# Optimization experiments

Hardware: AMD Instinct MI355X
Metric: run time of the kernel (lower is better)

Reference implementation:

```python
import jax, jax.numpy as jnp
import numpy as np

SAMPLE_SIZE = 4096  # deterministic mode: first SAMPLE_SIZE flattened pixels
EPS_STD = 1e-8
EPS_PDF = 1e-10


def _std(v):
    # torch.std is unbiased (ddof=1)
    return jnp.std(v, ddof=1)


def _adaptive_sigma(v):
    # sigma=None path: 0.2 * std, clamped to [0.001, 1.0]
    return jnp.clip(_std(v) * 0.2, 0.001, 1.0)


def _normalize(v):
    return (v - jnp.mean(v)) / (_std(v) + EPS_STD)


def _marginal_pdf(values, sigma):
    vn = _normalize(values)                      # [N]
    resid = vn[None, :] - vn[:, None]            # [N, N]
    kernel = jnp.exp(-0.5 * (resid / sigma) ** 2)
    pdf = jnp.mean(kernel, axis=1)               # [N]
    return pdf / (jnp.sum(pdf) + EPS_PDF)


def _joint_pdf(v1, v2, s1, s2):
    vn1 = _normalize(v1)
    vn2 = _normalize(v2)
    r1 = vn1[None, :] - vn1[:, None]             # [N, N]
    r2 = vn2[None, :] - vn2[:, None]             # [N, N]
    kernel = jnp.exp(-0.5 * (r1 / s1) ** 2) * jnp.exp(-0.5 * (r2 / s2) ** 2)
    pdf = jnp.mean(kernel, axis=1)
    return pdf / (jnp.sum(pdf) + EPS_PDF)


def _mi_kde(img1, img2):
    x = img1.reshape(-1)[:SAMPLE_SIZE]
    y = img2.reshape(-1)[:SAMPLE_SIZE]
    s1 = _adaptive_sigma(x)
    s2 = _adaptive_sigma(y)
    p1 = _marginal_pdf(x, s1)
    p2 = _marginal_pdf(y, s2)
    pj = _joint_pdf(x, y, s1, s2)
    ratio = (pj + EPS_PDF) / (p1 * p2 + EPS_PDF)
    log_ratio = jnp.log(jnp.clip(ratio, 1e-10, 1e10))
    return jnp.sum(pj * log_ratio)


def setup_inputs() -> dict:
    key = jax.random.key(0)
    k1, k2, k3 = jax.random.split(key, 3)
    shape = (2, 1, 128, 128)  # [B, C, H, W] images in [0, 1]
    return {
        "fused_img": jax.random.uniform(k1, shape, dtype=jnp.float32),
        "source_img1": jax.random.uniform(k2, shape, dtype=jnp.float32),
        "source_img2": jax.random.uniform(k3, shape, dtype=jnp.float32),
    }


def reference(fused_img, source_img1, source_img2):
    B = fused_img.shape[0]
    total = jnp.float32(0.0)
    for b in range(B):  # small fixed batch loop, matches original
        total = total + _mi_kde(fused_img[b], source_img1[b]) \
                      + _mi_kde(fused_img[b], source_img2[b])
    return -(total / B)
```

## Files before the change

### kernel.cpp

```cpp
#include <hip/hip_runtime.h>

#define N 4096
#define NBIN 1024
#define LOG2E 1.4426950408889634f

__device__ __forceinline__ float fast_exp2(float x) {
#if __has_builtin(__builtin_amdgcn_exp2f)
    return __builtin_amdgcn_exp2f(x);
#else
    return exp2f(x);
#endif
}

__device__ float block_reduce_sum(float v) {
    __shared__ float red[16];
    int lane = threadIdx.x & 63;
    int wid = threadIdx.x >> 6;
    #pragma unroll
    for (int off = 32; off; off >>= 1) v += __shfl_down(v, off, 64);
    if (lane == 0) red[wid] = v;
    __syncthreads();
    if (threadIdx.x == 0) {
        int nw = (int)(blockDim.x >> 6);
        float s = red[0];
        for (int w = 1; w < nw; ++w) s += red[w];
        red[0] = s;
    }
    __syncthreads();
    float r = red[0];
    __syncthreads();
    return r;
}

__device__ float4 block_reduce_stats(float s, float sq, float mn, float mx) {
    __shared__ float4 red4[16];
    int lane = threadIdx.x & 63;
    int wid = threadIdx.x >> 6;
    #pragma unroll
    for (int off = 32; off; off >>= 1) {
        s  += __shfl_down(s, off, 64);
        sq += __shfl_down(sq, off, 64);
        mn  = fminf(mn, __shfl_down(mn, off, 64));
        mx  = fmaxf(mx, __shfl_down(mx, off, 64));
    }
    if (lane == 0) red4[wid] = make_float4(s, sq, mn, mx);
    __syncthreads();
    if (threadIdx.x == 0) {
        float4 r = red4[0];
        #pragma unroll
        for (int w = 1; w < 16; ++w) {
            float4 q = red4[w];
            r.x += q.x; r.y += q.y;
            r.z = fminf(r.z, q.z); r.w = fmaxf(r.w, q.w);
        }
        red4[0] = r;
    }
    __syncthreads();
    float4 r = red4[0];
    __syncthreads();
    return r;
}

__global__ void __launch_bounds__(1024)
k_prep(const float* __restrict__ fused,
       const float* __restrict__ s1,
       const float* __restrict__ s2,
       float2* __restrict__ xa,
       float2* __restrict__ ma,
       float* __restrict__ par,
       float* __restrict__ hcnt,
       float* __restrict__ hmu) {
    __shared__ unsigned int cnt[NBIN];
    __shared__ int qs[NBIN];
    int vec = blockIdx.x;
    int b = vec / 3, k = vec % 3;
    const float* src = (k == 0 ? fused : (k == 1 ? s1 : s2)) + b * 16384;
    int tid = threadIdx.x;

    cnt[tid] = 0u; qs[tid] = 0;

    float v[4];
    float s = 0.f, sq = 0.f, mn = 1e30f, mx = -1e30f;
    #pragma unroll
    for (int t = 0; t < 4; ++t) {
        v[t] = src[tid + t * 1024];
        s += v[t]; sq = fmaf(v[t], v[t], sq);
        mn = fminf(mn, v[t]); mx = fmaxf(mx, v[t]);
    }
    float4 r = block_reduce_stats(s, sq, mn, mx);
    float mean = r.x * (1.0f / 4096.0f);
    float tssq = r.y - 4096.0f * mean * mean;
    float stdv = sqrtf(fmaxf(tssq, 0.f) / 4095.0f);
    float sigma = fminf(fmaxf(0.2f * stdv, 0.001f), 1.0f);
    float inv = 1.0f / (stdv + 1e-8f);
    float c1 = -0.5f * LOG2E / (sigma * sigma);
    float xmin = (r.z - mean) * inv;
    float xmax = (r.w - mean) * inv;
    float range = fmaxf(xmax - xmin, 1e-6f);
    float inv_bw = (float)NBIN / range;
    float binw = range * (1.0f / NBIN);

    float2* xav = xa + (size_t)vec * N;
    float2* mav = ma + (size_t)vec * N;
    __syncthreads();
    #pragma unroll
    for (int t = 0; t < 4; ++t) {
        int i = tid + t * 1024;
        float x = (v[t] - mean) * inv;
        float a = c1 * x * x;
        xav[i] = make_float2(x, a);
        mav[i] = make_float2(-2.0f * c1 * x, a);
        float rel = x - xmin;
        int bb = min(NBIN - 1, max(0, (int)(rel * inv_bw)));
        atomicAdd(&cnt[bb], 1u);
        atomicAdd(&qs[bb], (int)rintf(rel * 16384.0f));
    }
    __syncthreads();
    {
        unsigned int c = cnt[tid];
        hcnt[vec * NBIN + tid] = (float)c;
        float mu = c ? xmin + ((float)qs[tid] / (float)c) * (1.0f / 16384.0f)
                     : xmin + (tid + 0.5f) * binw;
        hmu[vec * NBIN + tid] = mu;
    }
    if (tid == 0) {
        par[vec * 8 + 0] = xmin;
        par[vec * 8 + 1] = inv_bw;
        par[vec * 8 + 2] = binw;
        par[vec * 8 + 3] = c1;
    }
}

__global__ void __launch_bounds__(256, 8)
k_main(const float2* __restrict__ xa,
       const float2* __restrict__ ma,
       const float* __restrict__ par,
       const float* __restrict__ hcnt,
       const float* __restrict__ hmu,
       float* __restrict__ marg,
       float* __restrict__ msum_part,
       float* __restrict__ part, int js) {
    __shared__ float4 sj[128];
    const int nib = 4;
    int bid = blockIdx.x;
    int tid = threadIdx.x;

    if (bid < 96) {
        int vec = bid >> 4, ic = bid & 15;
        int i = ic * 256 + tid;
        const float* P = par + vec * 8;
        float xmin = P[0], inv_bw = P[1], c1 = P[3];
        float xi = xa[(size_t)vec * N + i].x;
        float R = sqrtf(45.0f / fabsf(c1));
        int b0 = max(0, (int)((xi - R - xmin) * inv_bw));
        int b1 = min(NBIN - 1, (int)((xi + R - xmin) * inv_bw) + 1);
        const float* hc = hcnt + vec * NBIN;
        const float* hm = hmu + vec * NBIN;
        float acc = 0.f;
        #pragma unroll 4
        for (int bb = b0; bb <= b1; ++bb) {
            float d = xi - hm[bb];
            acc += hc[bb] * fast_exp2(c1 * d * d);
        }
        float raw = acc * (1.0f / N);
        marg[(size_t)vec * N + i] = raw;
        float tot = block_reduce_sum(raw);
        if (tid == 0) msum_part[bid] = tot;
        return;
    }

    int bid2 = bid - 96;
    int tt = bid2 / (nib * js);
    int rem = bid2 % (nib * js);
    int ib = rem / js, jsp = rem % js;
    int b = tt >> 1, pr = tt & 1;
    int vx = b * 3, vy = b * 3 + 1 + pr;
    int jlen = N / js;
    int j0 = jsp * jlen;
    int ibase = ib * 1024 + tid;

    const float2* xav = xa + (size_t)vx * N;
    const float2* yav = xa + (size_t)vy * N;
    const float2* mxv = ma + (size_t)vx * N;
    const float2* myv = ma + (size_t)vy * N;

    float mx[4], my[4], C[4];
    #pragma unroll
    for (int u = 0; u < 4; ++u) {
        float2 qx = mxv[ibase + u * 256];
        float2 qy = myv[ibase + u * 256];
        mx[u] = qx.x; my[u] = qy.x; C[u] = qx.y + qy.y;
    }
    float acc[4] = {0.f, 0.f, 0.f, 0.f};

    for (int jt = 0; jt < jlen; jt += 128) {
        int cnt = min(128, jlen - jt);
        __syncthreads();
        if (tid < cnt) {
            float2 xq = xav[j0 + jt + tid];
            float2 yq = yav[j0 + jt + tid];
            sj[tid] = make_float4(xq.x, yq.x, xq.y + yq.y, 0.f);
        }
        __syncthreads();
        #pragma unroll 2
        for (int j = 0; j < cnt; j += 2) {
            float4 q0 = sj[j];
            float4 q1 = sj[j + 1];
            float e0[4], e1[4], f0[4], f1[4];
            #pragma unroll
            for (int u = 0; u < 4; ++u) {
                e0[u] = fmaf(my[u], q0.y, fmaf(mx[u], q0.x, C[u])) + q0.z;
                e1[u] = fmaf(my[u], q1.y, fmaf(mx[u], q1.x, C[u])) + q1.z;
            }
            #pragma unroll
            for (int u = 0; u < 4; ++u) {
                f0[u] = fast_exp2(e0[u]);
                f1[u] = fast_exp2(e1[u]);
            }
            #pragma unroll
            for (int u = 0; u < 4; ++u)
                acc[u] += (f0[u] + f1[u]);
        }
    }
    float* dst = part + ((size_t)tt * js + jsp) * N + ibase;
    dst[0]   = acc[0];
    dst[256] = acc[1];
    dst[512] = acc[2];
    dst[768] = acc[3];
}

__global__ void k_reduce(const float* __restrict__ part,
                         const float* __restrict__ marg,
                         float* __restrict__ A_part,
                         float* __restrict__ jsum_part, int js) {
    int blk = blockIdx.x;
    int tt = blk >> 4;
    int ic = blk & 15;
    int b = tt >> 1, pr = tt & 1;
    int vx = b * 3, vy = b * 3 + 1 + pr;
    int i = ic * 256 + threadIdx.x;
    float s = 0.f;
    #pragma unroll 4
    for (int q = 0; q < js; ++q) s += part[((size_t)tt * js + q) * N + i];
    s *= (1.0f / N);
    float rx = marg[(size_t)vx * N + i];
    float ry = marg[(size_t)vy * N + i];
    float a = s * __logf(s / (rx * ry));
    float stot = block_reduce_sum(s);
    float atot = block_reduce_sum(a);
    if (threadIdx.x == 0) {
        jsum_part[blk] = stot;
        A_part[blk] = atot;
    }
}

__global__ void k_fin(const float* __restrict__ A_part,
                      const float* __restrict__ jsum_part,
                      const float* __restrict__ msum_part,
                      float* __restrict__ out) {
    __shared__ float svec[6], stask[4], sA[4];
    int tid = threadIdx.x;
    if (tid < 6) {
        float s = 0.f;
        #pragma unroll
        for (int q = 0; q < 16; ++q) s += msum_part[tid * 16 + q];
        svec[tid] = s;
    } else if (tid >= 8 && tid < 12) {
        int c = tid - 8;
        float s = 0.f, a = 0.f;
        #pragma unroll
        for (int q = 0; q < 16; ++q) {
            s += jsum_part[c * 16 + q];
            a += A_part[c * 16 + q];
        }
        stask[c] = s;
        sA[c] = a;
    }
    __syncthreads();
    if (tid == 0) {
        float mi = 0.f;
        #pragma unroll
        for (int c = 0; c < 4; ++c) {
            int b = c >> 1, pr = c & 1;
            int vx = b * 3, vy = b * 3 + 1 + pr;
            mi += sA[c] / stask[c] + __logf(svec[vx] * svec[vy] / stask[c]);
        }
        out[0] = -mi * 0.5f;
    }
}

extern "C" void kernel_launch(void* const* d_in, const int* in_sizes, int n_in,
                              void* d_out, int out_size, void* d_ws, size_t ws_size,
                              hipStream_t stream) {
    const float* fused = (const float*)d_in[0];
    const float* s1    = (const float*)d_in[1];
    const float* s2    = (const float*)d_in[2];
    float* out = (float*)d_out;
    float* ws  = (float*)d_ws;

    const size_t off_xa   = 0;
    const size_t off_ma   = off_xa + 12 * (size_t)N;
    const size_t off_par  = off_ma + 12 * (size_t)N;
    const size_t off_hc   = off_par + 64;
    const size_t off_hm   = off_hc + 6 * NBIN;
    const size_t off_mg   = off_hm + 6 * NBIN;
    const size_t off_ms   = off_mg + 6 * (size_t)N;
    const size_t off_A    = off_ms + 128;
    const size_t off_js   = off_A + 64;
    const size_t off_part = off_js + 64;

    int js = 32;
    while (js > 1 && (off_part + (size_t)4 * js * N) * 4 > ws_size) js >>= 1;

    float2* ws_xa  = (float2*)(ws + off_xa);
    float2* ws_ma  = (float2*)(ws + off_ma);
    float*  ws_par = ws + off_par;
    float*  ws_hc  = ws + off_hc;
    float*  ws_hm  = ws + off_hm;
    float*  ws_mg  = ws + off_mg;
    float*  ws_ms  = ws + off_ms;
    float*  ws_A   = ws + off_A;
    float*  ws_js  = ws + off_js;
    float*  ws_part = ws + off_part;

    k_prep<<<dim3(6), dim3(1024), 0, stream>>>(fused, s1, s2, ws_xa, ws_ma,
                                               ws_par, ws_hc, ws_hm);
    k_main<<<dim3(96 + 4 * 4 * js), dim3(256), 0, stream>>>(
        ws_xa, ws_ma, ws_par, ws_hc, ws_hm, ws_mg, ws_ms, ws_part, js);
    k_reduce<<<dim3(64), dim3(256), 0, stream>>>(ws_part, ws_mg, ws_A, ws_js, js);
    k_fin<<<dim3(1), dim3(128), 0, stream>>>(ws_A, ws_js, ws_ms, out);
}
```

Before: 33.02 us.

## Fuse final reduction into reduce kernel via last-block atomic counter; raise j-split

```diff
diff --git a/kernel.cpp b/kernel.cpp
--- a/kernel.cpp
+++ b/kernel.cpp
@@ -69,7 +69,8 @@
        float2* __restrict__ ma,
        float* __restrict__ par,
        float* __restrict__ hcnt,
-       float* __restrict__ hmu) {
+       float* __restrict__ hmu,
+       unsigned int* __restrict__ counter) {
     __shared__ unsigned int cnt[NBIN];
     __shared__ int qs[NBIN];
     int vec = blockIdx.x;
@@ -77,6 +78,7 @@
     const float* src = (k == 0 ? fused : (k == 1 ? s1 : s2)) + b * 16384;
     int tid = threadIdx.x;
 
+    if (vec == 0 && tid == 0) *counter = 0u;
     cnt[tid] = 0u; qs[tid] = 0;
 
     float v[4];
@@ -229,10 +231,15 @@
     dst[768] = acc[3];
 }
 
-__global__ void k_reduce(const float* __restrict__ part,
+__global__ void k_redfin(const float* __restrict__ part,
                          const float* __restrict__ marg,
+                         const float* __restrict__ msum_part,
                          float* __restrict__ A_part,
-                         float* __restrict__ jsum_part, int js) {
+                         float* __restrict__ jsum_part,
+                         unsigned int* __restrict__ counter,
+                         float* __restrict__ out, int js) {
+    __shared__ bool isLast;
+    __shared__ float svec[6], stask[4], sA[4];
     int blk = blockIdx.x;
     int tt = blk >> 4;
     int ic = blk & 15;
@@ -251,39 +258,39 @@
     if (threadIdx.x == 0) {
         jsum_part[blk] = stot;
         A_part[blk] = atot;
-    }
-}
-
-__global__ void k_fin(const float* __restrict__ A_part,
-                      const float* __restrict__ jsum_part,
-                      const float* __restrict__ msum_part,
-                      float* __restrict__ out) {
-    __shared__ float svec[6], stask[4], sA[4];
+        __threadfence();
+        unsigned int done = atomicAdd(counter, 1u);
+        isLast = (done == 63u);
+    }
+    __syncthreads();
+    if (!isLast) return;
+    __threadfence();
+
     int tid = threadIdx.x;
     if (tid < 6) {
-        float s = 0.f;
+        float ss = 0.f;
         #pragma unroll
-        for (int q = 0; q < 16; ++q) s += msum_part[tid * 16 + q];
-        svec[tid] = s;
+        for (int q = 0; q < 16; ++q) ss += msum_part[tid * 16 + q];
+        svec[tid] = ss;
     } else if (tid >= 8 && tid < 12) {
         int c = tid - 8;
-        float s = 0.f, a = 0.f;
+        float ss = 0.f, aa = 0.f;
         #pragma unroll
         for (int q = 0; q < 16; ++q) {
-            s += jsum_part[c * 16 + q];
-            a += A_part[c * 16 + q];
-        }
-        stask[c] = s;
-        sA[c] = a;
+            ss += jsum_part[c * 16 + q];
+            aa += A_part[c * 16 + q];
+        }
+        stask[c] = ss;
+        sA[c] = aa;
     }
     __syncthreads();
     if (tid == 0) {
         float mi = 0.f;
         #pragma unroll
         for (int c = 0; c < 4; ++c) {
-            int b = c >> 1, pr = c & 1;
-            int vx = b * 3, vy = b * 3 + 1 + pr;
-            mi += sA[c] / stask[c] + __logf(svec[vx] * svec[vy] / stask[c]);
+            int bb = c >> 1, pp = c & 1;
+            int wx = bb * 3, wy = bb * 3 + 1 + pp;
+            mi += sA[c] / stask[c] + __logf(svec[wx] * svec[wy] / stask[c]);
         }
         out[0] = -mi * 0.5f;
     }
@@ -307,9 +314,10 @@
     const size_t off_ms   = off_mg + 6 * (size_t)N;
     const size_t off_A    = off_ms + 128;
     const size_t off_js   = off_A + 64;
-    const size_t off_part = off_js + 64;
-
-    int js = 32;
+    const size_t off_ctr  = off_js + 64;
+    const size_t off_part = off_ctr + 16;
+
+    int js = 128;
     while (js > 1 && (off_part + (size_t)4 * js * N) * 4 > ws_size) js >>= 1;
 
     float2* ws_xa  = (float2*)(ws + off_xa);
@@ -321,12 +329,13 @@
     float*  ws_ms  = ws + off_ms;
     float*  ws_A   = ws + off_A;
     float*  ws_js  = ws + off_js;
+    unsigned int* ws_ctr = (unsigned int*)(ws + off_ctr);
     float*  ws_part = ws + off_part;
 
     k_prep<<<dim3(6), dim3(1024), 0, stream>>>(fused, s1, s2, ws_xa, ws_ma,
-                                               ws_par, ws_hc, ws_hm);
+                                               ws_par, ws_hc, ws_hm, ws_ctr);
     k_main<<<dim3(96 + 4 * 4 * js), dim3(256), 0, stream>>>(
         ws_xa, ws_ma, ws_par, ws_hc, ws_hm, ws_mg, ws_ms, ws_part, js);
-    k_reduce<<<dim3(64), dim3(256), 0, stream>>>(ws_part, ws_mg, ws_A, ws_js, js);
-    k_fin<<<dim3(1), dim3(128), 0, stream>>>(ws_A, ws_js, ws_ms, out);
-}
+    k_redfin<<<dim3(64), dim3(256), 0, stream>>>(ws_part, ws_mg, ws_ms,
+                                                 ws_A, ws_js, ws_ctr, out, js);
+}
```

Measured after the change: 43.07 us. 1.3x slower.
